# Kernel tuning notes

Hardware: AMD Instinct MI355X
Metric: run time of the kernel (lower is better)

## Reference

```python
import jax, jax.numpy as jnp
import numpy as np

EPS = 1e-12  # torch F.normalize eps


def _l2norm(v, axis):
    n = jnp.sqrt(jnp.sum(v * v, axis=axis, keepdims=True))
    return v / jnp.maximum(n, EPS)


def setup_inputs() -> dict:
    key = jax.random.key(0)
    k1, k2, k3 = jax.random.split(key, 3)
    N, D, H, W, K = 64, 256, 64, 64, 64
    x = jax.random.normal(k1, (N, D, H, W), dtype=jnp.float32)
    conv_weight = jax.random.normal(k2, (K, D), dtype=jnp.float32)
    centroids = jax.random.uniform(k3, (K, D), dtype=jnp.float32)
    return {"x": x, "conv_weight": conv_weight, "centroids": centroids}


def reference(x, conv_weight, centroids):
    # x: [N, D, H, W]; conv_weight: [K, D] (1x1 conv); centroids: [K, D]
    N, D, H, W = x.shape
    K = centroids.shape[0]
    x = _l2norm(x, axis=1)                       # descriptor-wise L2 norm over D
    xf = x.reshape(N, D, H * W)                  # [N, D, L]
    # 1x1 conv == matmul over channel dim: [N, K, L]
    logits = jnp.einsum('kd,ndl->nkl', conv_weight, xf)
    a = jax.nn.softmax(logits, axis=1)           # softmax over clusters
    # vlad[n,k,d] = sum_l a[n,k,l] * (x[n,d,l] - c[k,d])
    #            = (a @ x^T)[n,k,d] - (sum_l a[n,k,l]) * c[k,d]
    vlad = jnp.einsum('nkl,ndl->nkd', a, xf) - a.sum(axis=2)[:, :, None] * centroids[None]
    vlad = _l2norm(vlad, axis=2)                 # intra-normalization
    vlad = vlad.reshape(N, K * D)
    vlad = _l2norm(vlad, axis=1)                 # global L2 norm
    return vlad
```

## Files before the change

kernel.cpp:

```cpp
#include <hip/hip_runtime.h>

typedef unsigned short u16;
typedef unsigned int u32;
typedef short bf16x8 __attribute__((ext_vector_type(8)));
typedef float f32x4  __attribute__((ext_vector_type(4)));

#define NN 64
#define DD 256
#define LL 4096
#define KK 64
#define CHUNK 512
#define SUB 32
#define NSTEP 16
#define NCH 8
#define SSZ (KK*DD)
#define XLD_S 264
#define XDL_S 40
#define AKL_S 40

__device__ __forceinline__ u16 f2bf(float f) {
  union { float f; u32 i; } v; v.f = f;
  return (u16)((v.i + 0x8000u) >> 16);
}

__device__ __forceinline__ void barrier_lds() {
  asm volatile("s_waitcnt lgkmcnt(0)\n\ts_barrier" ::: "memory");
}

__global__ void zero_ws_kernel(float* __restrict__ p, int n4) {
  int i = blockIdx.x * 256 + threadIdx.x;
  if (i < n4) ((f32x4*)p)[i] = (f32x4){0.f, 0.f, 0.f, 0.f};
}

template <bool PARTIAL>
__global__ __launch_bounds__(256, 2) void netvlad_main(
    const float* __restrict__ xg, const float* __restrict__ wg,
    float* __restrict__ Sg, float* __restrict__ Ag) {
  __shared__ __align__(16) u16 x_ld[SUB * XLD_S];
  __shared__ __align__(16) u16 x_dl[4][64 * XDL_S];
  __shared__ __align__(16) u16 akl[KK * AKL_S];
  __shared__ float pnw[4][SUB];
  __shared__ float wsum[4][SUB];

  const int tid  = threadIdx.x;
  const int w    = tid >> 6;
  const int lane = tid & 63;
  const int quad = lane >> 4;
  const int l15  = lane & 15;
  const int g    = lane >> 3;
  const int c    = lane & 7;
  const int n    = blockIdx.x >> 3;
  const int ch   = blockIdx.x & 7;

  bf16x8 aw[8];
  {
    const float* wp = wg + (w * 16 + l15) * DD + quad * 8;
#pragma unroll
    for (int s = 0; s < 8; ++s) {
      f32x4 wa = *(const f32x4*)(wp + s * 32);
      f32x4 wb = *(const f32x4*)(wp + s * 32 + 4);
      bf16x8 t;
#pragma unroll
      for (int j = 0; j < 4; ++j) { t[j] = (short)f2bf(wa[j]); t[j + 4] = (short)f2bf(wb[j]); }
      aw[s] = t;
    }
  }

  f32x4 acc2[4][4];
#pragma unroll
  for (int a = 0; a < 4; ++a)
#pragma unroll
    for (int b = 0; b < 4; ++b) acc2[a][b] = (f32x4){0.f, 0.f, 0.f, 0.f};
  float regAk[4] = {0.f, 0.f, 0.f, 0.f};

  const float* xw = xg + (size_t)n * DD * LL + (size_t)(w * 64 + g * 8) * LL
                    + ch * CHUNK + c * 4;

  f32x4 buf0[8], buf1[8];
#pragma unroll
  for (int i = 0; i < 8; ++i) buf0[i] = *(const f32x4*)(xw + (size_t)i * LL);

  auto step = [&](f32x4 (&cur)[8], f32x4 (&nxt)[8], int s) {
    if (s + 1 < NSTEP) {
      const float* q = xw + (s + 1) * SUB;
#pragma unroll
      for (int i = 0; i < 8; ++i) nxt[i] = *(const f32x4*)(q + (size_t)i * LL);
    }

    {
      f32x4 pj = (f32x4){0.f, 0.f, 0.f, 0.f};
#pragma unroll
      for (int i = 0; i < 8; ++i) pj += cur[i] * cur[i];
#pragma unroll
      for (int o = 8; o <= 32; o <<= 1)
#pragma unroll
        for (int j = 0; j < 4; ++j) pj[j] += __shfl_xor(pj[j], o);
      if (g == 0) *(f32x4*)&pnw[w][c * 4] = pj;
    }

    u16 xb[8][4];
#pragma unroll
    for (int i = 0; i < 8; ++i)
#pragma unroll
      for (int j = 0; j < 4; ++j) xb[i][j] = f2bf(cur[i][j]);
#pragma unroll
    for (int i = 0; i < 8; ++i) {
      u32 lo = (u32)xb[i][0] | ((u32)xb[i][1] << 16);
      u32 hi = (u32)xb[i][2] | ((u32)xb[i][3] << 16);
      *(uint2*)&x_dl[w][(g * 8 + i) * XDL_S + c * 4] = make_uint2(lo, hi);
    }
#pragma unroll
    for (int j = 0; j < 4; ++j) {
      bf16x8 col;
#pragma unroll
      for (int i = 0; i < 8; ++i) col[i] = (short)xb[i][j];
      *(bf16x8*)&x_ld[(c * 4 + j) * XLD_S + w * 64 + g * 8] = col;
    }
    barrier_lds();

    f32x4 acc1[2];
    acc1[0] = (f32x4){0.f, 0.f, 0.f, 0.f};
    acc1[1] = (f32x4){0.f, 0.f, 0.f, 0.f};
#pragma unroll
    for (int s8 = 0; s8 < 8; ++s8)
#pragma unroll
      for (int lt = 0; lt < 2; ++lt) {
        bf16x8 b = *(const bf16x8*)&x_ld[(lt * 16 + l15) * XLD_S + s8 * 32 + quad * 8];
        acc1[lt] = __builtin_amdgcn_mfma_f32_16x16x32_bf16(aw[s8], b, acc1[lt], 0, 0, 0);
      }
    float rno[2], e[2][4], ps[2];
#pragma unroll
    for (int lt = 0; lt < 2; ++lt) {
      int col = lt * 16 + l15;
      float s4 = pnw[0][col] + pnw[1][col] + pnw[2][col] + pnw[3][col];
      rno[lt] = rsqrtf(fmaxf(s4, 1e-24f));
      float p = 0.f;
#pragma unroll
      for (int r = 0; r < 4; ++r) { e[lt][r] = __expf(acc1[lt][r] * rno[lt]); p += e[lt][r]; }
      p += __shfl_xor(p, 16);
      p += __shfl_xor(p, 32);
      ps[lt] = p;
    }
    if (quad < 2) wsum[w][quad * 16 + l15] = (quad == 0) ? ps[0] : ps[1];
    barrier_lds();

#pragma unroll
    for (int lt = 0; lt < 2; ++lt) {
      int col = lt * 16 + l15;
      float rs = 1.f / (wsum[0][col] + wsum[1][col] + wsum[2][col] + wsum[3][col]);
      float rr = rs * rno[lt];
#pragma unroll
      for (int r = 0; r < 4; ++r) {
        regAk[r] += e[lt][r] * rs;
        akl[(w * 16 + quad * 4 + r) * AKL_S + col] = f2bf(e[lt][r] * rr);
      }
    }
    barrier_lds();

    bf16x8 bx[4];
#pragma unroll
    for (int dt = 0; dt < 4; ++dt)
      bx[dt] = *(const bf16x8*)&x_dl[w][(dt * 16 + l15) * XDL_S + quad * 8];
#pragma unroll
    for (int kt = 0; kt < 4; ++kt) {
      bf16x8 aA = *(const bf16x8*)&akl[(kt * 16 + l15) * AKL_S + quad * 8];
#pragma unroll
      for (int dt = 0; dt < 4; ++dt)
        acc2[kt][dt] = __builtin_amdgcn_mfma_f32_16x16x32_bf16(aA, bx[dt], acc2[kt][dt], 0, 0, 0);
    }
    barrier_lds();
  };

#pragma unroll 1
  for (int sp = 0; sp < NSTEP / 2; ++sp) {
    step(buf0, buf1, 2 * sp);
    step(buf1, buf0, 2 * sp + 1);
  }

  if (PARTIAL) {
    float* Sp = Sg + (size_t)blockIdx.x * SSZ;
#pragma unroll
    for (int kt = 0; kt < 4; ++kt)
#pragma unroll
      for (int dt = 0; dt < 4; ++dt)
#pragma unroll
        for (int r = 0; r < 4; ++r)
          Sp[(kt * 16 + quad * 4 + r) * DD + w * 64 + dt * 16 + l15] = acc2[kt][dt][r];
  } else {
    float* Sn = Sg + (size_t)n * SSZ;
#pragma unroll
    for (int kt = 0; kt < 4; ++kt)
#pragma unroll
      for (int dt = 0; dt < 4; ++dt)
#pragma unroll
        for (int r = 0; r < 4; ++r)
          atomicAdd(&Sn[(kt * 16 + quad * 4 + r) * DD + w * 64 + dt * 16 + l15],
                    acc2[kt][dt][r]);
  }
#pragma unroll
  for (int o = 1; o <= 8; o <<= 1)
#pragma unroll
    for (int r = 0; r < 4; ++r) regAk[r] += __shfl_xor(regAk[r], o);
  if (l15 == 0) {
    if (PARTIAL) {
      float* Ap = Ag + (size_t)blockIdx.x * KK;
#pragma unroll
      for (int r = 0; r < 4; ++r) Ap[w * 16 + quad * 4 + r] = regAk[r];
    } else {
#pragma unroll
      for (int r = 0; r < 4; ++r) atomicAdd(&Ag[n * KK + w * 16 + quad * 4 + r], regAk[r]);
    }
  }
}

template <int NSL>
__global__ __launch_bounds__(256, 2) void netvlad_fin(
    const float* __restrict__ Sg, const float* __restrict__ Ag,
    const float* __restrict__ cg, float* __restrict__ outg) {
  __shared__ float wtot[4];
  const int n = blockIdx.x, tid = threadIdx.x;
  const int w = tid >> 6, lane = tid & 63;
  const float* Sb = Sg + (size_t)n * NSL * SSZ;
  const float* Ab = Ag + (size_t)n * NSL * KK;

  f32x4 v[16];
  float rk[16];
  float tot = 0.f;
#pragma unroll
  for (int i = 0; i < 16; ++i) {
    const int k = w * 16 + i;
    float Ak = 0.f;
#pragma unroll
    for (int sl = 0; sl < NSL; ++sl) Ak += Ab[sl * KK + k];
    f32x4 sacc = (f32x4){0.f, 0.f, 0.f, 0.f};
#pragma unroll
    for (int sl = 0; sl < NSL; ++sl)
      sacc += *(const f32x4*)&Sb[(size_t)sl * SSZ + k * DD + lane * 4];
    f32x4 c4 = *(const f32x4*)&cg[k * DD + lane * 4];
    f32x4 t = sacc - Ak * c4;
    v[i] = t;
    float q = t[0] * t[0] + t[1] * t[1] + t[2] * t[2] + t[3] * t[3];
#pragma unroll
    for (int o = 1; o <= 32; o <<= 1) q += __shfl_xor(q, o);
    float r = 1.f / fmaxf(sqrtf(q), 1e-12f);
    rk[i] = r;
    tot += q * r * r;
  }
  if (lane == 0) wtot[w] = tot;
  __syncthreads();
  const float gtot = wtot[0] + wtot[1] + wtot[2] + wtot[3];
  const float gs = 1.f / fmaxf(sqrtf(gtot), 1e-12f);
#pragma unroll
  for (int i = 0; i < 16; ++i) {
    const int k = w * 16 + i;
    const float sc = rk[i] * gs;
    f32x4 o = v[i];
    o[0] *= sc; o[1] *= sc; o[2] *= sc; o[3] *= sc;
    *(f32x4*)&outg[(size_t)n * SSZ + k * DD + lane * 4] = o;
  }
}

extern "C" void kernel_launch(void* const* d_in, const int* in_sizes, int n_in,
                              void* d_out, int out_size, void* d_ws, size_t ws_size,
                              hipStream_t stream) {
  const float* x   = (const float*)d_in[0];
  const float* wgt = (const float*)d_in[1];
  const float* cen = (const float*)d_in[2];
  float* out = (float*)d_out;

  const size_t nblk = (size_t)NN * NCH;
  const size_t need = nblk * SSZ * 4 + nblk * KK * 4;
  if (ws_size >= need) {
    float* Sp = (float*)d_ws;
    float* Ap = Sp + nblk * SSZ;
    hipLaunchKernelGGL((netvlad_main<true>), dim3(NN * NCH), dim3(256), 0, stream, x, wgt, Sp, Ap);
    hipLaunchKernelGGL((netvlad_fin<NCH>), dim3(NN), dim3(256), 0, stream, Sp, Ap, cen, out);
  } else {
    float* S = (float*)d_ws;
    float* A = S + (size_t)NN * SSZ;
    const int n4 = (NN * SSZ + NN * KK) / 4;
    hipLaunchKernelGGL(zero_ws_kernel, dim3((n4 + 255) / 256), dim3(256), 0, stream, S, n4);
    hipLaunchKernelGGL((netvlad_main<false>), dim3(NN * NCH), dim3(256), 0, stream, x, wgt, S, A);
    hipLaunchKernelGGL((netvlad_fin<1>), dim3(NN), dim3(256), 0, stream, S, A, cen, out);
  }
}
```

Baseline: 395.7 us.

## Move softmax denominator into x columns to drop two LDS barriers per step

The per-column softmax denominator is now applied to the bf16 x_dl tile instead of the assignment tile. This lets the assignment tile be written before the partial-sum barrier, and the trailing barrier is replaced by a local LDS wait, leaving two barriers per step instead of four. Separately, the finalize kernel is widened from 256 to 1024 threads per block, so each wave handles 4 clusters instead of 16. The cost is an extra vector read of the partial sums and rescaling of x before bf16 rounding. Correctness now depends on the reordered LDS write/read hazards across steps still being covered by the remaining barriers.

```diff
diff --git a/kernel.cpp b/kernel.cpp
--- a/kernel.cpp
+++ b/kernel.cpp
@@ -98,23 +98,19 @@
       if (g == 0) *(f32x4*)&pnw[w][c * 4] = pj;
     }
 
-    u16 xb[8][4];
-#pragma unroll
-    for (int i = 0; i < 8; ++i)
-#pragma unroll
-      for (int j = 0; j < 4; ++j) xb[i][j] = f2bf(cur[i][j]);
-#pragma unroll
-    for (int i = 0; i < 8; ++i) {
-      u32 lo = (u32)xb[i][0] | ((u32)xb[i][1] << 16);
-      u32 hi = (u32)xb[i][2] | ((u32)xb[i][3] << 16);
-      *(uint2*)&x_dl[w][(g * 8 + i) * XDL_S + c * 4] = make_uint2(lo, hi);
-    }
-#pragma unroll
-    for (int j = 0; j < 4; ++j) {
-      bf16x8 col;
-#pragma unroll
-      for (int i = 0; i < 8; ++i) col[i] = (short)xb[i][j];
-      *(bf16x8*)&x_ld[(c * 4 + j) * XLD_S + w * 64 + g * 8] = col;
+    {
+      u16 xb[8][4];
+#pragma unroll
+      for (int i = 0; i < 8; ++i)
+#pragma unroll
+        for (int j = 0; j < 4; ++j) xb[i][j] = f2bf(cur[i][j]);
+#pragma unroll
+      for (int j = 0; j < 4; ++j) {
+        bf16x8 col;
+#pragma unroll
+        for (int i = 0; i < 8; ++i) col[i] = (short)xb[i][j];
+        *(bf16x8*)&x_ld[(c * 4 + j) * XLD_S + w * 64 + g * 8] = col;
+      }
     }
     barrier_lds();
 
@@ -128,18 +124,21 @@
         bf16x8 b = *(const bf16x8*)&x_ld[(lt * 16 + l15) * XLD_S + s8 * 32 + quad * 8];
         acc1[lt] = __builtin_amdgcn_mfma_f32_16x16x32_bf16(aw[s8], b, acc1[lt], 0, 0, 0);
       }
-    float rno[2], e[2][4], ps[2];
+    float e[2][4], ps[2];
 #pragma unroll
     for (int lt = 0; lt < 2; ++lt) {
       int col = lt * 16 + l15;
       float s4 = pnw[0][col] + pnw[1][col] + pnw[2][col] + pnw[3][col];
-      rno[lt] = rsqrtf(fmaxf(s4, 1e-24f));
+      float rno = rsqrtf(fmaxf(s4, 1e-24f));
       float p = 0.f;
 #pragma unroll
-      for (int r = 0; r < 4; ++r) { e[lt][r] = __expf(acc1[lt][r] * rno[lt]); p += e[lt][r]; }
+      for (int r = 0; r < 4; ++r) { e[lt][r] = __expf(acc1[lt][r] * rno); p += e[lt][r]; }
       p += __shfl_xor(p, 16);
       p += __shfl_xor(p, 32);
       ps[lt] = p;
+#pragma unroll
+      for (int r = 0; r < 4; ++r)
+        akl[(w * 16 + quad * 4 + r) * AKL_S + col] = f2bf(e[lt][r] * rno);
     }
     if (quad < 2) wsum[w][quad * 16 + l15] = (quad == 0) ? ps[0] : ps[1];
     barrier_lds();
@@ -148,14 +147,25 @@
     for (int lt = 0; lt < 2; ++lt) {
       int col = lt * 16 + l15;
       float rs = 1.f / (wsum[0][col] + wsum[1][col] + wsum[2][col] + wsum[3][col]);
-      float rr = rs * rno[lt];
-#pragma unroll
-      for (int r = 0; r < 4; ++r) {
-        regAk[r] += e[lt][r] * rs;
-        akl[(w * 16 + quad * 4 + r) * AKL_S + col] = f2bf(e[lt][r] * rr);
+#pragma unroll
+      for (int r = 0; r < 4; ++r) regAk[r] += e[lt][r] * rs;
+    }
+    {
+      f32x4 den = *(const f32x4*)&wsum[0][c * 4];
+      den += *(const f32x4*)&wsum[1][c * 4];
+      den += *(const f32x4*)&wsum[2][c * 4];
+      den += *(const f32x4*)&wsum[3][c * 4];
+      f32x4 rs4;
+#pragma unroll
+      for (int j = 0; j < 4; ++j) rs4[j] = 1.f / den[j];
+#pragma unroll
+      for (int i = 0; i < 8; ++i) {
+        u32 lo = (u32)f2bf(cur[i][0] * rs4[0]) | ((u32)f2bf(cur[i][1] * rs4[1]) << 16);
+        u32 hi = (u32)f2bf(cur[i][2] * rs4[2]) | ((u32)f2bf(cur[i][3] * rs4[3]) << 16);
+        *(uint2*)&x_dl[w][(g * 8 + i) * XDL_S + c * 4] = make_uint2(lo, hi);
       }
     }
-    barrier_lds();
+    asm volatile("s_waitcnt lgkmcnt(0)" ::: "memory");
 
     bf16x8 bx[4];
 #pragma unroll
@@ -168,7 +178,6 @@
       for (int dt = 0; dt < 4; ++dt)
         acc2[kt][dt] = __builtin_amdgcn_mfma_f32_16x16x32_bf16(aA, bx[dt], acc2[kt][dt], 0, 0, 0);
     }
-    barrier_lds();
   };
 
 #pragma unroll 1
@@ -214,21 +223,21 @@
 }
 
 template <int NSL>
-__global__ __launch_bounds__(256, 2) void netvlad_fin(
+__global__ __launch_bounds__(1024, 1) void netvlad_fin(
     const float* __restrict__ Sg, const float* __restrict__ Ag,
     const float* __restrict__ cg, float* __restrict__ outg) {
-  __shared__ float wtot[4];
+  __shared__ float wtot[16];
   const int n = blockIdx.x, tid = threadIdx.x;
   const int w = tid >> 6, lane = tid & 63;
   const float* Sb = Sg + (size_t)n * NSL * SSZ;
   const float* Ab = Ag + (size_t)n * NSL * KK;
 
-  f32x4 v[16];
-  float rk[16];
+  f32x4 v[4];
+  float rk[4];
   float tot = 0.f;
 #pragma unroll
-  for (int i = 0; i < 16; ++i) {
-    const int k = w * 16 + i;
+  for (int i = 0; i < 4; ++i) {
+    const int k = w * 4 + i;
     float Ak = 0.f;
 #pragma unroll
     for (int sl = 0; sl < NSL; ++sl) Ak += Ab[sl * KK + k];
@@ -248,11 +257,13 @@
   }
   if (lane == 0) wtot[w] = tot;
   __syncthreads();
-  const float gtot = wtot[0] + wtot[1] + wtot[2] + wtot[3];
+  float gtot = 0.f;
+#pragma unroll
+  for (int u = 0; u < 16; ++u) gtot += wtot[u];
   const float gs = 1.f / fmaxf(sqrtf(gtot), 1e-12f);
 #pragma unroll
-  for (int i = 0; i < 16; ++i) {
-    const int k = w * 16 + i;
+  for (int i = 0; i < 4; ++i) {
+    const int k = w * 4 + i;
     const float sc = rk[i] * gs;
     f32x4 o = v[i];
     o[0] *= sc; o[1] *= sc; o[2] *= sc; o[3] *= sc;
@@ -274,13 +285,13 @@
     float* Sp = (float*)d_ws;
     float* Ap = Sp + nblk * SSZ;
     hipLaunchKernelGGL((netvlad_main<true>), dim3(NN * NCH), dim3(256), 0, stream, x, wgt, Sp, Ap);
-    hipLaunchKernelGGL((netvlad_fin<NCH>), dim3(NN), dim3(256), 0, stream, Sp, Ap, cen, out);
+    hipLaunchKernelGGL((netvlad_fin<NCH>), dim3(NN), dim3(1024), 0, stream, Sp, Ap, cen, out);
   } else {
     float* S = (float*)d_ws;
     float* A = S + (size_t)NN * SSZ;
     const int n4 = (NN * SSZ + NN * KK) / 4;
     hipLaunchKernelGGL(zero_ws_kernel, dim3((n4 + 255) / 256), dim3(256), 0, stream, S, n4);
     hipLaunchKernelGGL((netvlad_main<false>), dim3(NN * NCH), dim3(256), 0, stream, x, wgt, S, A);
-    hipLaunchKernelGGL((netvlad_fin<1>), dim3(NN), dim3(256), 0, stream, S, A, cen, out);
-  }
-}
+    hipLaunchKernelGGL((netvlad_fin<1>), dim3(NN), dim3(1024), 0, stream, S, A, cen, out);
+  }
+}
```

Result: no change. 393.3 us (-0.6%).
